# Performance work log

Hardware: AMD Instinct MI355X
Metric: run time of the kernel (lower is better)

The kernel has to match this reference:

```python
import jax, jax.numpy as jnp
import numpy as np

N_RAYS = 131072
N_SAMPLES = 128
BIG_DIST = 1e10  # sentinel last-interval distance, as in the torch code
EPS = 1e-10


def setup_inputs() -> dict:
    key = jax.random.key(0)
    k1, k2, k3 = jax.random.split(key, 3)
    raw = jax.random.normal(k1, (N_RAYS, N_SAMPLES, 4), dtype=jnp.float32)
    # integration depths must be sorted along the sample axis; typical near/far = [2, 6]
    z_vals = jnp.sort(
        jax.random.uniform(k2, (N_RAYS, N_SAMPLES), dtype=jnp.float32, minval=2.0, maxval=6.0),
        axis=-1,
    )
    rays_d = jax.random.normal(k3, (N_RAYS, 3), dtype=jnp.float32)
    return {"raw": raw, "z_vals": z_vals, "rays_d": rays_d}


def reference(raw, z_vals, rays_d):
    # distances between adjacent samples; last interval is 'infinite'
    dists = z_vals[..., 1:] - z_vals[..., :-1]                       # [R, S-1]
    dists = jnp.concatenate(
        [dists, jnp.full(dists[..., :1].shape, BIG_DIST, dists.dtype)], axis=-1
    )                                                                # [R, S]
    dists = dists * jnp.linalg.norm(rays_d, axis=-1, keepdims=True)  # scale by |d|

    rgb = jax.nn.sigmoid(raw[..., :3])                               # [R, S, 3]
    sigma = jax.nn.relu(raw[..., 3])                                 # raw_noise_std = 0
    alpha = 1.0 - jnp.exp(-sigma * dists)                            # [R, S]

    # exclusive cumprod of transmittance: T_i = prod_{j<i} (1 - alpha_j + eps)
    trans = jnp.cumprod(
        jnp.concatenate([jnp.ones_like(alpha[:, :1]), 1.0 - alpha + EPS], axis=-1),
        axis=-1,
    )[:, :-1]                                                        # [R, S]
    weights = alpha * trans                                          # [R, S]

    rgb_map = jnp.sum(weights[..., None] * rgb, axis=-2)             # [R, 3]
    depth_map = jnp.sum(weights * z_vals, axis=-1)                   # [R]
    acc_map = jnp.sum(weights, axis=-1)                              # [R]
    disp_map = 1.0 / jnp.maximum(EPS, depth_map / acc_map)           # [R]
    # white_bkgd = False, so no background compositing
    return rgb_map, disp_map, acc_map, weights, depth_map
```

## Files before the change

kernel.cpp:

```cpp
#include <hip/hip_runtime.h>
#include <math.h>

#define N_RAYS    131072
#define N_SAMPLES 128
#define BIG_DIST  1e10f
#define EPS       1e-10f

#define OFF_RGB    0
#define OFF_DISP   393216
#define OFF_ACC    524288
#define OFF_W      655360
#define OFF_DEPTH  17432576

__global__ __launch_bounds__(256) void nerf_render_scan_kernel(
    const float4* __restrict__ raw,
    const float*  __restrict__ z_vals,
    const float*  __restrict__ rays_d,
    float* __restrict__ out)
{
    const int tid  = blockIdx.x * blockDim.x + threadIdx.x;
    const int r    = tid >> 6;
    const int lane = threadIdx.x & 63;
    if (r >= N_RAYS) return;

    const float4* rawr = raw + (size_t)r * N_SAMPLES;
    const float4  rv0 = rawr[2 * lane];
    const float4  rv1 = rawr[2 * lane + 1];

    const float2* zr2 = (const float2*)(z_vals + (size_t)r * N_SAMPLES);
    const float2  z   = zr2[lane];

    const float znext = __shfl_down(z.x, 1);

    const float dxx = rays_d[3 * r + 0];
    const float dyy = rays_d[3 * r + 1];
    const float dzz = rays_d[3 * r + 2];
    const float nrm = sqrtf(dxx * dxx + dyy * dyy + dzz * dzz);

    const float dist0 = (z.y - z.x) * nrm;
    const float dist1 = (lane == 63) ? (BIG_DIST * nrm) : ((znext - z.y) * nrm);

    const float sig0 = fmaxf(rv0.w, 0.0f);
    const float sig1 = fmaxf(rv1.w, 0.0f);
    const float a0 = 1.0f - __expf(-sig0 * dist0);
    const float a1 = 1.0f - __expf(-sig1 * dist1);

    const float f0 = 1.0f - a0 + EPS;
    const float f1 = 1.0f - a1 + EPS;
    const float p  = f0 * f1;

    float sp = p;
#pragma unroll
    for (int off = 1; off < 64; off <<= 1) {
        const float t = __shfl_up(sp, off);
        sp *= (lane >= off) ? t : 1.0f;
    }
    float Texc = __shfl_up(sp, 1);
    if (lane == 0) Texc = 1.0f;

    const float T0 = Texc;
    const float T1 = Texc * f0;
    const float w0 = a0 * T0;
    const float w1 = a1 * T1;

    ((float2*)(out + OFF_W + (size_t)r * N_SAMPLES))[lane] = make_float2(w0, w1);

    const float sr0 = __builtin_amdgcn_rcpf(1.0f + __expf(-rv0.x));
    const float sg0 = __builtin_amdgcn_rcpf(1.0f + __expf(-rv0.y));
    const float sb0 = __builtin_amdgcn_rcpf(1.0f + __expf(-rv0.z));
    const float sr1 = __builtin_amdgcn_rcpf(1.0f + __expf(-rv1.x));
    const float sg1 = __builtin_amdgcn_rcpf(1.0f + __expf(-rv1.y));
    const float sb1 = __builtin_amdgcn_rcpf(1.0f + __expf(-rv1.z));

    float cr    = w0 * sr0 + w1 * sr1;
    float cg    = w0 * sg0 + w1 * sg1;
    float cb    = w0 * sb0 + w1 * sb1;
    float depth = w0 * z.x + w1 * z.y;
    float acc   = w0 + w1;

#pragma unroll
    for (int m = 32; m > 0; m >>= 1) {
        cr    += __shfl_xor(cr, m);
        cg    += __shfl_xor(cg, m);
        cb    += __shfl_xor(cb, m);
        depth += __shfl_xor(depth, m);
        acc   += __shfl_xor(acc, m);
    }

    if (lane == 0) {
        out[OFF_RGB + 3 * r + 0] = cr;
        out[OFF_RGB + 3 * r + 1] = cg;
        out[OFF_RGB + 3 * r + 2] = cb;
        out[OFF_ACC + r]   = acc;
        out[OFF_DEPTH + r] = depth;
        out[OFF_DISP + r]  = 1.0f / fmaxf(EPS, depth / acc);
    }
}

extern "C" void kernel_launch(void* const* d_in, const int* in_sizes, int n_in,
                              void* d_out, int out_size, void* d_ws, size_t ws_size,
                              hipStream_t stream) {
    const float4* raw    = (const float4*)d_in[0];
    const float*  z_vals = (const float*)d_in[1];
    const float*  rays_d = (const float*)d_in[2];
    float* out = (float*)d_out;

    const int block = 256;
    const int rays_per_block = block / 64;
    const int grid = N_RAYS / rays_per_block;
    nerf_render_scan_kernel<<<grid, block, 0, stream>>>(raw, z_vals, rays_d, out);
}
```

Before: 410.1 us.

## Use persistent waves with register double-buffered prefetch of next ray

Launches a fixed set of waves that each loop over many rays, loading the next ray's raw samples, depths and direction into registers while the current ray is processed. Lanes now own samples lane and lane+64 instead of an adjacent pair, so two parallel scans are run and combined using the first half's total product. This is meant to hide global load latency behind the scan and reduction work. In exchange it adds shuffle work, uses more registers, and gives less wave-level parallelism.

```diff
diff --git a/kernel.cpp b/kernel.cpp
--- a/kernel.cpp
+++ b/kernel.cpp
@@ -12,88 +12,127 @@
 #define OFF_W      655360
 #define OFF_DEPTH  17432576
 
-__global__ __launch_bounds__(256) void nerf_render_scan_kernel(
+#define NWAVES        8192
+#define RAYS_PER_WAVE (N_RAYS / NWAVES)
+
+__global__ __launch_bounds__(256) void nerf_render_persist(
     const float4* __restrict__ raw,
     const float*  __restrict__ z_vals,
     const float*  __restrict__ rays_d,
     float* __restrict__ out)
 {
-    const int tid  = blockIdx.x * blockDim.x + threadIdx.x;
-    const int r    = tid >> 6;
+    const int wid  = (blockIdx.x * blockDim.x + threadIdx.x) >> 6;
     const int lane = threadIdx.x & 63;
-    if (r >= N_RAYS) return;
 
-    const float4* rawr = raw + (size_t)r * N_SAMPLES;
-    const float4  rv0 = rawr[2 * lane];
-    const float4  rv1 = rawr[2 * lane + 1];
+    float4 rvA[2], rvB[2];
+    float  zA[2],  zB[2];
+    float  rdx[2], rdy[2], rdz[2];
 
-    const float2* zr2 = (const float2*)(z_vals + (size_t)r * N_SAMPLES);
-    const float2  z   = zr2[lane];
+    {
+        const int r = wid;
+        const float4* rawr = raw + (size_t)r * N_SAMPLES;
+        rvA[0] = rawr[lane];
+        rvB[0] = rawr[64 + lane];
+        const float* zr = z_vals + (size_t)r * N_SAMPLES;
+        zA[0] = zr[lane];
+        zB[0] = zr[64 + lane];
+        const int ru = __builtin_amdgcn_readfirstlane(r);
+        rdx[0] = rays_d[3 * ru + 0];
+        rdy[0] = rays_d[3 * ru + 1];
+        rdz[0] = rays_d[3 * ru + 2];
+    }
 
-    const float znext = __shfl_down(z.x, 1);
+#pragma unroll 2
+    for (int i = 0; i < RAYS_PER_WAVE; ++i) {
+        const int cur = i & 1;
+        const int nxt = cur ^ 1;
 
-    const float dxx = rays_d[3 * r + 0];
-    const float dyy = rays_d[3 * r + 1];
-    const float dzz = rays_d[3 * r + 2];
-    const float nrm = sqrtf(dxx * dxx + dyy * dyy + dzz * dzz);
+        if (i + 1 < RAYS_PER_WAVE) {
+            const int rn = wid + (i + 1) * NWAVES;
+            const float4* rawr = raw + (size_t)rn * N_SAMPLES;
+            rvA[nxt] = rawr[lane];
+            rvB[nxt] = rawr[64 + lane];
+            const float* zr = z_vals + (size_t)rn * N_SAMPLES;
+            zA[nxt] = zr[lane];
+            zB[nxt] = zr[64 + lane];
+            const int ru = __builtin_amdgcn_readfirstlane(rn);
+            rdx[nxt] = rays_d[3 * ru + 0];
+            rdy[nxt] = rays_d[3 * ru + 1];
+            rdz[nxt] = rays_d[3 * ru + 2];
+        }
 
-    const float dist0 = (z.y - z.x) * nrm;
-    const float dist1 = (lane == 63) ? (BIG_DIST * nrm) : ((znext - z.y) * nrm);
+        const int r = wid + i * NWAVES;
+        const float4 ra = rvA[cur];
+        const float4 rb = rvB[cur];
+        const float  za = zA[cur];
+        const float  zb = zB[cur];
+        const float  dxx = rdx[cur], dyy = rdy[cur], dzz = rdz[cur];
+        const float  nrm = sqrtf(dxx * dxx + dyy * dyy + dzz * dzz);
 
-    const float sig0 = fmaxf(rv0.w, 0.0f);
-    const float sig1 = fmaxf(rv1.w, 0.0f);
-    const float a0 = 1.0f - __expf(-sig0 * dist0);
-    const float a1 = 1.0f - __expf(-sig1 * dist1);
+        const float zsA = __shfl_down(za, 1);
+        const float zb0 = __shfl(zb, 0);
+        const float zsB = __shfl_down(zb, 1);
+        const float znA = (lane == 63) ? zb0 : zsA;
 
-    const float f0 = 1.0f - a0 + EPS;
-    const float f1 = 1.0f - a1 + EPS;
-    const float p  = f0 * f1;
+        const float distA = (znA - za) * nrm;
+        const float distB = (lane == 63) ? (BIG_DIST * nrm) : ((zsB - zb) * nrm);
 
-    float sp = p;
+        const float sigA = fmaxf(ra.w, 0.0f);
+        const float sigB = fmaxf(rb.w, 0.0f);
+        const float aA = 1.0f - __expf(-sigA * distA);
+        const float aB = 1.0f - __expf(-sigB * distB);
+        const float fA = 1.0f - aA + EPS;
+        const float fB = 1.0f - aB + EPS;
+
+        float sA = fA, sB = fB;
 #pragma unroll
-    for (int off = 1; off < 64; off <<= 1) {
-        const float t = __shfl_up(sp, off);
-        sp *= (lane >= off) ? t : 1.0f;
-    }
-    float Texc = __shfl_up(sp, 1);
-    if (lane == 0) Texc = 1.0f;
+        for (int off = 1; off < 64; off <<= 1) {
+            const float tA = __shfl_up(sA, off);
+            const float tB = __shfl_up(sB, off);
+            if (lane >= off) { sA *= tA; sB *= tB; }
+        }
+        float TA  = __shfl_up(sA, 1); if (lane == 0) TA  = 1.0f;
+        float TBe = __shfl_up(sB, 1); if (lane == 0) TBe = 1.0f;
+        const float Ph = __shfl(sA, 63);
+        const float TB = Ph * TBe;
 
-    const float T0 = Texc;
-    const float T1 = Texc * f0;
-    const float w0 = a0 * T0;
-    const float w1 = a1 * T1;
+        const float wA = aA * TA;
+        const float wB = aB * TB;
 
-    ((float2*)(out + OFF_W + (size_t)r * N_SAMPLES))[lane] = make_float2(w0, w1);
+        float* wout = out + OFF_W + (size_t)r * N_SAMPLES;
+        wout[lane]      = wA;
+        wout[64 + lane] = wB;
 
-    const float sr0 = __builtin_amdgcn_rcpf(1.0f + __expf(-rv0.x));
-    const float sg0 = __builtin_amdgcn_rcpf(1.0f + __expf(-rv0.y));
-    const float sb0 = __builtin_amdgcn_rcpf(1.0f + __expf(-rv0.z));
-    const float sr1 = __builtin_amdgcn_rcpf(1.0f + __expf(-rv1.x));
-    const float sg1 = __builtin_amdgcn_rcpf(1.0f + __expf(-rv1.y));
-    const float sb1 = __builtin_amdgcn_rcpf(1.0f + __expf(-rv1.z));
+        const float srA = __builtin_amdgcn_rcpf(1.0f + __expf(-ra.x));
+        const float sgA = __builtin_amdgcn_rcpf(1.0f + __expf(-ra.y));
+        const float sbA = __builtin_amdgcn_rcpf(1.0f + __expf(-ra.z));
+        const float srB = __builtin_amdgcn_rcpf(1.0f + __expf(-rb.x));
+        const float sgB = __builtin_amdgcn_rcpf(1.0f + __expf(-rb.y));
+        const float sbB = __builtin_amdgcn_rcpf(1.0f + __expf(-rb.z));
 
-    float cr    = w0 * sr0 + w1 * sr1;
-    float cg    = w0 * sg0 + w1 * sg1;
-    float cb    = w0 * sb0 + w1 * sb1;
-    float depth = w0 * z.x + w1 * z.y;
-    float acc   = w0 + w1;
+        float cr    = wA * srA + wB * srB;
+        float cg    = wA * sgA + wB * sgB;
+        float cb    = wA * sbA + wB * sbB;
+        float depth = wA * za  + wB * zb;
+        float acc   = wA + wB;
 
 #pragma unroll
-    for (int m = 32; m > 0; m >>= 1) {
-        cr    += __shfl_xor(cr, m);
-        cg    += __shfl_xor(cg, m);
-        cb    += __shfl_xor(cb, m);
-        depth += __shfl_xor(depth, m);
-        acc   += __shfl_xor(acc, m);
-    }
+        for (int m = 32; m > 0; m >>= 1) {
+            cr    += __shfl_xor(cr, m);
+            cg    += __shfl_xor(cg, m);
+            cb    += __shfl_xor(cb, m);
+            depth += __shfl_xor(depth, m);
+            acc   += __shfl_xor(acc, m);
+        }
 
-    if (lane == 0) {
-        out[OFF_RGB + 3 * r + 0] = cr;
-        out[OFF_RGB + 3 * r + 1] = cg;
-        out[OFF_RGB + 3 * r + 2] = cb;
-        out[OFF_ACC + r]   = acc;
-        out[OFF_DEPTH + r] = depth;
-        out[OFF_DISP + r]  = 1.0f / fmaxf(EPS, depth / acc);
+        if (lane == 0) {
+            out[OFF_RGB + 3 * r + 0] = cr;
+            out[OFF_RGB + 3 * r + 1] = cg;
+            out[OFF_RGB + 3 * r + 2] = cb;
+            out[OFF_ACC + r]   = acc;
+            out[OFF_DEPTH + r] = depth;
+            out[OFF_DISP + r]  = 1.0f / fmaxf(EPS, depth / acc);
+        }
     }
 }
 
@@ -106,7 +145,6 @@
     float* out = (float*)d_out;
 
     const int block = 256;
-    const int rays_per_block = block / 64;
-    const int grid = N_RAYS / rays_per_block;
-    nerf_render_scan_kernel<<<grid, block, 0, stream>>>(raw, z_vals, rays_d, out);
+    const int grid  = NWAVES * 64 / block;
+    nerf_render_persist<<<grid, block, 0, stream>>>(raw, z_vals, rays_d, out);
 }
```

Measured after the change: 436.2 us. +6.4%, slower.

## Process four rays per wavefront to interleave scans and loads for ILP

Applied to the files above, without the earlier changes.

Each wavefront now handles four rays instead of one. It issues all their loads up front and interleaves the shuffle-based prefix-product scans and reductions across the four rays. The goal is to hide load latency and the serial dependency chains of the shuffle scans with more independent work per wave. In exchange the grid is four times smaller and register use is higher, which may lower occupancy.

```diff
diff --git a/kernel.cpp b/kernel.cpp
--- a/kernel.cpp
+++ b/kernel.cpp
@@ -12,88 +12,113 @@
 #define OFF_W      655360
 #define OFF_DEPTH  17432576
 
-__global__ __launch_bounds__(256) void nerf_render_scan_kernel(
+#define RPW 4
+
+__global__ __launch_bounds__(256) void nerf_render_ilp4(
     const float4* __restrict__ raw,
     const float*  __restrict__ z_vals,
     const float*  __restrict__ rays_d,
     float* __restrict__ out)
 {
-    const int tid  = blockIdx.x * blockDim.x + threadIdx.x;
-    const int r    = tid >> 6;
-    const int lane = threadIdx.x & 63;
-    if (r >= N_RAYS) return;
+    const int wid   = (blockIdx.x * blockDim.x + threadIdx.x) >> 6;
+    const int lane  = threadIdx.x & 63;
+    const int rbase = wid * RPW;
 
-    const float4* rawr = raw + (size_t)r * N_SAMPLES;
-    const float4  rv0 = rawr[2 * lane];
-    const float4  rv1 = rawr[2 * lane + 1];
+    float4 rv0[RPW], rv1[RPW];
+    float2 z[RPW];
+#pragma unroll
+    for (int k = 0; k < RPW; ++k) {
+        const size_t r = rbase + k;
+        const float4* rawr = raw + r * N_SAMPLES;
+        rv0[k] = rawr[2 * lane];
+        rv1[k] = rawr[2 * lane + 1];
+        z[k]   = ((const float2*)(z_vals + r * N_SAMPLES))[lane];
+    }
+    float nrm[RPW];
+#pragma unroll
+    for (int k = 0; k < RPW; ++k) {
+        const int r = rbase + k;
+        const float dxx = rays_d[3 * r + 0];
+        const float dyy = rays_d[3 * r + 1];
+        const float dzz = rays_d[3 * r + 2];
+        nrm[k] = sqrtf(dxx * dxx + dyy * dyy + dzz * dzz);
+    }
 
-    const float2* zr2 = (const float2*)(z_vals + (size_t)r * N_SAMPLES);
-    const float2  z   = zr2[lane];
+    float a0[RPW], a1[RPW], f0[RPW], sp[RPW];
+#pragma unroll
+    for (int k = 0; k < RPW; ++k) {
+        const float znext = __shfl_down(z[k].x, 1);
+        const float dist0 = (z[k].y - z[k].x) * nrm[k];
+        const float dist1 = (lane == 63) ? (BIG_DIST * nrm[k])
+                                         : ((znext - z[k].y) * nrm[k]);
+        const float sig0 = fmaxf(rv0[k].w, 0.0f);
+        const float sig1 = fmaxf(rv1[k].w, 0.0f);
+        a0[k] = 1.0f - __expf(-sig0 * dist0);
+        a1[k] = 1.0f - __expf(-sig1 * dist1);
+        f0[k] = 1.0f - a0[k] + EPS;
+        const float f1 = 1.0f - a1[k] + EPS;
+        sp[k] = f0[k] * f1;
+    }
 
-    const float znext = __shfl_down(z.x, 1);
-
-    const float dxx = rays_d[3 * r + 0];
-    const float dyy = rays_d[3 * r + 1];
-    const float dzz = rays_d[3 * r + 2];
-    const float nrm = sqrtf(dxx * dxx + dyy * dyy + dzz * dzz);
-
-    const float dist0 = (z.y - z.x) * nrm;
-    const float dist1 = (lane == 63) ? (BIG_DIST * nrm) : ((znext - z.y) * nrm);
-
-    const float sig0 = fmaxf(rv0.w, 0.0f);
-    const float sig1 = fmaxf(rv1.w, 0.0f);
-    const float a0 = 1.0f - __expf(-sig0 * dist0);
-    const float a1 = 1.0f - __expf(-sig1 * dist1);
-
-    const float f0 = 1.0f - a0 + EPS;
-    const float f1 = 1.0f - a1 + EPS;
-    const float p  = f0 * f1;
-
-    float sp = p;
 #pragma unroll
     for (int off = 1; off < 64; off <<= 1) {
-        const float t = __shfl_up(sp, off);
-        sp *= (lane >= off) ? t : 1.0f;
+        float t[RPW];
+#pragma unroll
+        for (int k = 0; k < RPW; ++k) t[k] = __shfl_up(sp[k], off);
+#pragma unroll
+        for (int k = 0; k < RPW; ++k) if (lane >= off) sp[k] *= t[k];
     }
-    float Texc = __shfl_up(sp, 1);
-    if (lane == 0) Texc = 1.0f;
 
-    const float T0 = Texc;
-    const float T1 = Texc * f0;
-    const float w0 = a0 * T0;
-    const float w1 = a1 * T1;
+    float cr[RPW], cg[RPW], cb[RPW], depth[RPW], acc[RPW];
+#pragma unroll
+    for (int k = 0; k < RPW; ++k) {
+        float Texc = __shfl_up(sp[k], 1);
+        if (lane == 0) Texc = 1.0f;
+        const float T0 = Texc;
+        const float T1 = Texc * f0[k];
+        const float w0 = a0[k] * T0;
+        const float w1 = a1[k] * T1;
 
-    ((float2*)(out + OFF_W + (size_t)r * N_SAMPLES))[lane] = make_float2(w0, w1);
+        const size_t r = rbase + k;
+        ((float2*)(out + OFF_W + r * N_SAMPLES))[lane] = make_float2(w0, w1);
 
-    const float sr0 = __builtin_amdgcn_rcpf(1.0f + __expf(-rv0.x));
-    const float sg0 = __builtin_amdgcn_rcpf(1.0f + __expf(-rv0.y));
-    const float sb0 = __builtin_amdgcn_rcpf(1.0f + __expf(-rv0.z));
-    const float sr1 = __builtin_amdgcn_rcpf(1.0f + __expf(-rv1.x));
-    const float sg1 = __builtin_amdgcn_rcpf(1.0f + __expf(-rv1.y));
-    const float sb1 = __builtin_amdgcn_rcpf(1.0f + __expf(-rv1.z));
+        const float sr0 = __builtin_amdgcn_rcpf(1.0f + __expf(-rv0[k].x));
+        const float sg0 = __builtin_amdgcn_rcpf(1.0f + __expf(-rv0[k].y));
+        const float sb0 = __builtin_amdgcn_rcpf(1.0f + __expf(-rv0[k].z));
+        const float sr1 = __builtin_amdgcn_rcpf(1.0f + __expf(-rv1[k].x));
+        const float sg1 = __builtin_amdgcn_rcpf(1.0f + __expf(-rv1[k].y));
+        const float sb1 = __builtin_amdgcn_rcpf(1.0f + __expf(-rv1[k].z));
 
-    float cr    = w0 * sr0 + w1 * sr1;
-    float cg    = w0 * sg0 + w1 * sg1;
-    float cb    = w0 * sb0 + w1 * sb1;
-    float depth = w0 * z.x + w1 * z.y;
-    float acc   = w0 + w1;
+        cr[k]    = w0 * sr0 + w1 * sr1;
+        cg[k]    = w0 * sg0 + w1 * sg1;
+        cb[k]    = w0 * sb0 + w1 * sb1;
+        depth[k] = w0 * z[k].x + w1 * z[k].y;
+        acc[k]   = w0 + w1;
+    }
 
 #pragma unroll
     for (int m = 32; m > 0; m >>= 1) {
-        cr    += __shfl_xor(cr, m);
-        cg    += __shfl_xor(cg, m);
-        cb    += __shfl_xor(cb, m);
-        depth += __shfl_xor(depth, m);
-        acc   += __shfl_xor(acc, m);
+#pragma unroll
+        for (int k = 0; k < RPW; ++k) {
+            cr[k]    += __shfl_xor(cr[k], m);
+            cg[k]    += __shfl_xor(cg[k], m);
+            cb[k]    += __shfl_xor(cb[k], m);
+            depth[k] += __shfl_xor(depth[k], m);
+            acc[k]   += __shfl_xor(acc[k], m);
+        }
     }
 
     if (lane == 0) {
-        out[OFF_RGB + 3 * r + 0] = cr;
-        out[OFF_RGB + 3 * r + 1] = cg;
-        out[OFF_RGB + 3 * r + 2] = cb;
-        out[OFF_ACC + r]   = acc;
-        out[OFF_DEPTH + r] = depth;
-        out[OFF_DISP + r]  = 1.0f / fmaxf(EPS, depth / acc);
+#pragma unroll
+        for (int k = 0; k < RPW; ++k) {
+            const size_t r = rbase + k;
+            out[OFF_RGB + 3 * r + 0] = cr[k];
+            out[OFF_RGB + 3 * r + 1] = cg[k];
+            out[OFF_RGB + 3 * r + 2] = cb[k];
+            out[OFF_ACC + r]   = acc[k];
+            out[OFF_DEPTH + r] = depth[k];
+            out[OFF_DISP + r]  = 1.0f / fmaxf(EPS, depth[k] / acc[k]);
+        }
     }
 }
 
@@ -106,7 +131,7 @@
     float* out = (float*)d_out;
 
     const int block = 256;
-    const int rays_per_block = block / 64;
-    const int grid = N_RAYS / rays_per_block;
-    nerf_render_scan_kernel<<<grid, block, 0, stream>>>(raw, z_vals, rays_d, out);
+    const int waves = N_RAYS / RPW;
+    const int grid  = waves * 64 / block;
+    nerf_render_ilp4<<<grid, block, 0, stream>>>(raw, z_vals, rays_d, out);
 }
```

Result: no change. 415.0 us (+1.2%).
